# Performance work log

Measured on AMD Instinct MI355X. Metric: run time of the kernel, lower is better.

Reference implementation:

```python
import jax, jax.numpy as jnp
import numpy as np

B, L, C, K = 8, 16384, 64, 7
NORM_FACTOR = 1.0
LN_EPS = 1e-6


def setup_inputs() -> dict:
    key = jax.random.key(0)
    k0, k1, k2 = jax.random.split(key, 3)
    x = jax.random.normal(k0, (B, L, C), dtype=jnp.float32)
    # lecun_normal-style init for (C_out, C_in, K) dynamic-conv weights
    weights = jax.random.normal(k1, (C, C, K), dtype=jnp.float32) / np.float32(np.sqrt(C))
    ln_scale = jnp.ones((C,), dtype=jnp.float32)
    ln_bias = jnp.zeros((C,), dtype=jnp.float32)
    conv_kernel = jax.random.normal(k2, (C, C), dtype=jnp.float32) / np.float32(np.sqrt(C))
    conv_bias = jnp.zeros((C,), dtype=jnp.float32)
    prelu_slope = jnp.asarray(0.01, dtype=jnp.float32)
    return {"x": x, "weights": weights, "ln_scale": ln_scale, "ln_bias": ln_bias,
            "conv_kernel": conv_kernel, "conv_bias": conv_bias, "prelu_slope": prelu_slope}


def reference(x, weights, ln_scale, ln_bias, conv_kernel, conv_bias, prelu_slope):
    b, l, c = x.shape
    k = weights.shape[-1]
    x0 = x  # residual source, (B, L, C)

    # im2col unfold over sequence: window 2K, stride 2, no padding
    p = jax.lax.conv_general_dilated_patches(
        jnp.transpose(x, (0, 2, 1)),  # (B, C, L)
        filter_shape=(2 * k,), window_strides=(2,), padding=((0, 0),))
    t = p.shape[-1]  # out_len = (L - 2K)//2 + 1
    p = jnp.reshape(p, (b, c, 2 * k, t))
    p = jnp.transpose(p, (0, 1, 3, 2))  # (B, C, T, 2K)

    # dynamic weights from the trailing 2T inputs: (B, 2T, C) x (C, C, K) -> (B, C, 2T, K)
    w = jnp.einsum('blc,dck->bdlk', x0[:, -(t * 2):, :], weights)
    even_seq = w[:, :, ::2, :]   # (B, C, T, K)
    odd_seq = w[:, :, 1::2, :]   # (B, C, T, K)
    w = jnp.stack([even_seq, odd_seq], axis=-1)         # (B, C, T, K, 2)
    w = jnp.reshape(w, (b, c, t, k * 2))                # interleaved (B, C, T, 2K)
    w = jnp.tanh(w / NORM_FACTOR)

    # gated windowed sum
    y = jnp.sum(p * w, axis=3)          # (B, C, T)
    y = jnp.transpose(y, (0, 2, 1))     # (B, T, C)

    # inner skip: stride-2 subsample of input, aligned to the tail
    y = x0[:, ::2, :][:, -t:, :] + y

    # LayerNorm over channel dim (flax default eps=1e-6, with scale and bias)
    mu = jnp.mean(y, axis=-1, keepdims=True)
    var = jnp.mean(jnp.square(y - mu), axis=-1, keepdims=True)
    yn = (y - mu) * jax.lax.rsqrt(var + LN_EPS) * ln_scale + ln_bias

    # 1x1 conv + PReLU + outer skip
    z = jnp.einsum('btc,co->bto', yn, conv_kernel) + conv_bias
    z = jnp.where(z >= 0, z, prelu_slope * z)
    return yn + z
```

## Files before the change

### kernel.cpp

```cpp
#include <hip/hip_runtime.h>
#include <stdint.h>

#define BB 8
#define LLEN 16384
#define CC 64
#define TOUT 8186
#define TILE_T 32
#define NROWS 76
#define SXS 68
#define SXGS 72
#define YNS 66
#define YNBS 72

typedef __attribute__((ext_vector_type(8))) short short8;
typedef __attribute__((ext_vector_type(4))) float float4v;
typedef __attribute__((ext_vector_type(4))) unsigned short ushort4v;

__device__ inline unsigned short f2bf(float f) {
  union { float f; uint32_t u; } v; v.f = f;
  uint32_t r = v.u + 0x7fffu + ((v.u >> 16) & 1u);
  return (unsigned short)(r >> 16);
}
__device__ inline float rcp_fast(float x) {
  float r;
  asm("v_rcp_f32 %0, %1" : "=v"(r) : "v"(x));
  return r;
}
__device__ inline float tanh_fast(float a) {
  float e = __expf(2.0f * a);
  return 1.0f - 2.0f * rcp_fast(e + 1.0f);
}

__global__ void prep_frags(const float* __restrict__ weights,
                           const float* __restrict__ ck,
                           unsigned short* __restrict__ wfrag,
                           unsigned short* __restrict__ ckfrag)
{
  int bid = blockIdx.x, tid = threadIdx.x;
  if (bid < 56) {
    int nt = bid >> 1, kh = bid & 1;
    for (int e = tid; e < 512; e += 256) {
      int ln = e >> 3, j = e & 7;
      int kk = nt >> 2;
      int d  = (nt & 3) * 16 + (ln & 15);
      int cp = kh * 32 + (ln >> 4) * 8 + j;
      wfrag[(bid * 64 + ln) * 8 + j] = f2bf(weights[d * 448 + cp * 7 + kk]);
    }
  } else {
    int bb2 = bid - 56;
    int nt = bb2 >> 1, kh = bb2 & 1;
    for (int e = tid; e < 512; e += 256) {
      int ln = e >> 3, j = e & 7;
      int oo = nt * 16 + (ln & 15);
      int c2 = kh * 32 + (ln >> 4) * 8 + j;
      ckfrag[(bb2 * 64 + ln) * 8 + j] = f2bf(ck[c2 * 64 + oo]);
    }
  }
}

__global__ __launch_bounds__(256, 4)
void convblock_main(const float* __restrict__ x,
                    const unsigned short* __restrict__ wfrag,
                    const unsigned short* __restrict__ ckfrag,
                    const float* __restrict__ ln_scale,
                    const float* __restrict__ ln_bias,
                    const float* __restrict__ conv_bias,
                    const float* __restrict__ prelu_slope,
                    float* __restrict__ out)
{
  __shared__ __align__(16) char smem[29888];
  float*          sx2 = (float*)smem;
  unsigned short* ynb = (unsigned short*)smem;
  unsigned short* sxg = (unsigned short*)(smem + 20672);
  float*          ynf = (float*)(smem + 20672);

  const int tid  = threadIdx.x;
  const int b    = blockIdx.x >> 8;
  const int t0   = (blockIdx.x & 255) * TILE_T;
  const int lane = tid & 63;
  const int w    = tid >> 6;
  const int l15  = tid & 15;
  const int q    = (tid >> 4) & 3;

  {
    const float* xb = x + (size_t)b * ((size_t)LLEN * CC);
    #pragma unroll
    for (int i = 0; i < 5; ++i) {
      int idx = tid + i * 256;
      if (idx < NROWS * 16) {
        int row = idx >> 4, f4 = idx & 15, c0 = f4 * 4;
        int rowg = 2 * t0 + row;
        if (rowg > LLEN - 1) rowg = LLEN - 1;
        float4v v = *(const float4v*)(xb + (size_t)rowg * CC + c0);
        int base = row * SXS + 16 * (f4 & 3) + (f4 >> 2);
        sx2[base + 0]  = v[0];
        sx2[base + 4]  = v[1];
        sx2[base + 8]  = v[2];
        sx2[base + 12] = v[3];
        if (row >= 12) {
          ushort4v p;
          p[0] = f2bf(v[0]); p[1] = f2bf(v[1]); p[2] = f2bf(v[2]); p[3] = f2bf(v[3]);
          *(ushort4v*)&sxg[(row - 12) * SXGS + c0] = p;
        }
      }
    }
  }
  float lnS[4], lnB[4];
  #pragma unroll
  for (int dq = 0; dq < 4; ++dq) {
    lnS[dq] = ln_scale[16 * dq + l15];
    lnB[dq] = ln_bias[16 * dq + l15];
  }
  __syncthreads();

  short8 a0 = *(const short8*)&sxg[(16 * w + l15) * SXGS + q * 8];
  short8 a1 = *(const short8*)&sxg[(16 * w + l15) * SXGS + 32 + q * 8];
  __syncthreads();

  float y[2][4];
  #pragma unroll
  for (int dlt = 0; dlt < 2; ++dlt)
    #pragma unroll
    for (int dq = 0; dq < 4; ++dq) y[dlt][dq] = 0.f;

  const int dtbase = 8 * w + 2 * q;
  #pragma unroll
  for (int kk = 0; kk < 7; ++kk) {
    float4v acc[4];
    #pragma unroll
    for (int dq = 0; dq < 4; ++dq) {
      int nt = kk * 4 + dq;
      short8 b0 = *(const short8*)&wfrag[((nt * 2 + 0) * 64 + lane) * 8];
      short8 b1 = *(const short8*)&wfrag[((nt * 2 + 1) * 64 + lane) * 8];
      float4v a = (float4v){0.f, 0.f, 0.f, 0.f};
      a = __builtin_amdgcn_mfma_f32_16x16x32_bf16(a0, b0, a, 0, 0, 0);
      a = __builtin_amdgcn_mfma_f32_16x16x32_bf16(a1, b1, a, 0, 0, 0);
      acc[dq] = a;
    }
    #pragma unroll
    for (int dlt = 0; dlt < 2; ++dlt) {
      int rowe = 2 * (dtbase + dlt) + 2 * kk;
      float4v xe = *(const float4v*)&sx2[rowe * SXS + l15 * 4];
      float4v xo = *(const float4v*)&sx2[(rowe + 1) * SXS + l15 * 4];
      #pragma unroll
      for (int dq = 0; dq < 4; ++dq) {
        float ge = tanh_fast(acc[dq][2 * dlt + 0]);
        float go = tanh_fast(acc[dq][2 * dlt + 1]);
        y[dlt][dq] += xe[dq] * ge + xo[dq] * go;
        if (kk == 6) y[dlt][dq] += xe[dq];
      }
    }
  }

  float ynr[2][4];
  #pragma unroll
  for (int dlt = 0; dlt < 2; ++dlt) {
    float s1 = y[dlt][0] + y[dlt][1] + y[dlt][2] + y[dlt][3];
    float s2 = y[dlt][0]*y[dlt][0] + y[dlt][1]*y[dlt][1]
             + y[dlt][2]*y[dlt][2] + y[dlt][3]*y[dlt][3];
    #pragma unroll
    for (int m = 1; m < 16; m <<= 1) {
      s1 += __shfl_xor(s1, m, 64);
      s2 += __shfl_xor(s2, m, 64);
    }
    float mu   = s1 * (1.0f / 64.0f);
    float var  = s2 * (1.0f / 64.0f) - mu * mu;
    float rstd = rsqrtf(var + 1e-6f);
    int dt = dtbase + dlt;
    #pragma unroll
    for (int dq = 0; dq < 4; ++dq) {
      float yn = (y[dlt][dq] - mu) * rstd * lnS[dq] + lnB[dq];
      ynr[dlt][dq] = yn;
      ynf[dt * YNS + 16 * dq + l15] = yn;
    }
  }
  __syncthreads();

  #pragma unroll
  for (int dlt = 0; dlt < 2; ++dlt)
    #pragma unroll
    for (int dq = 0; dq < 4; ++dq)
      ynb[(dtbase + dlt) * YNBS + 16 * dq + l15] = f2bf(ynr[dlt][dq]);
  __syncthreads();

  const float sl = prelu_slope[0];
  const int   o  = 16 * w + l15;
  const float cb = conv_bias[o];
  short8 bf0 = *(const short8*)&ckfrag[((w * 2 + 0) * 64 + lane) * 8];
  short8 bf1 = *(const short8*)&ckfrag[((w * 2 + 1) * 64 + lane) * 8];
  #pragma unroll
  for (int mt = 0; mt < 2; ++mt) {
    short8 af0 = *(const short8*)&ynb[(mt * 16 + l15) * YNBS + q * 8];
    short8 af1 = *(const short8*)&ynb[(mt * 16 + l15) * YNBS + 32 + q * 8];
    float4v zc = (float4v){0.f, 0.f, 0.f, 0.f};
    zc = __builtin_amdgcn_mfma_f32_16x16x32_bf16(af0, bf0, zc, 0, 0, 0);
    zc = __builtin_amdgcn_mfma_f32_16x16x32_bf16(af1, bf1, zc, 0, 0, 0);
    #pragma unroll
    for (int r = 0; r < 4; ++r) {
      int t  = mt * 16 + 4 * q + r;
      int tg = t0 + t;
      if (tg < TOUT) {
        float z = zc[r] + cb;
        z = (z >= 0.f) ? z : sl * z;
        out[((size_t)b * TOUT + tg) * CC + o] = ynf[t * YNS + o] + z;
      }
    }
  }
}

extern "C" void kernel_launch(void* const* d_in, const int* in_sizes, int n_in,
                              void* d_out, int out_size, void* d_ws, size_t ws_size,
                              hipStream_t stream)
{
  const float* x        = (const float*)d_in[0];
  const float* weights  = (const float*)d_in[1];
  const float* ln_scale = (const float*)d_in[2];
  const float* ln_bias  = (const float*)d_in[3];
  const float* ck       = (const float*)d_in[4];
  const float* cb       = (const float*)d_in[5];
  const float* slope    = (const float*)d_in[6];
  unsigned short* wfrag  = (unsigned short*)d_ws;
  unsigned short* ckfrag = (unsigned short*)((char*)d_ws + 57344);

  prep_frags<<<64, 256, 0, stream>>>(weights, ck, wfrag, ckfrag);
  convblock_main<<<BB * 256, 256, 0, stream>>>(x, wfrag, ckfrag, ln_scale,
                                               ln_bias, cb, slope, (float*)d_out);
}
```

Before: 112.8 us.

## Double tile to 64 outputs, stage weight fragments in LDS, pack bf16 pairs

Doubles the per-block time tile to 64 outputs, so each weight fragment now feeds two MFMA row groups, which halves the global weight-fragment traffic per output. Weight fragments are prefetched into a double-buffered LDS area with direct global-to-LDS loads, with a barrier after each tap. The fp32 x window in LDS is replaced by packed bf16 even/odd pairs in an XOR-swizzled layout to cut LDS size and bank conflicts. The costs are lower gated-sum precision from bf16 x, more LDS per block and fewer blocks per SM (launch bounds drop from 4 to 3), plus seven extra barriers.

```diff
diff --git a/kernel.cpp b/kernel.cpp
--- a/kernel.cpp
+++ b/kernel.cpp
@@ -5,15 +5,17 @@
 #define LLEN 16384
 #define CC 64
 #define TOUT 8186
-#define TILE_T 32
-#define NROWS 76
-#define SXS 68
-#define SXGS 72
+#define TILE_T 64
+#define NROWS 140
+#define NPAIR 70
+#define SXPS 68
+#define SXGS 68
 #define YNS 66
-#define YNBS 72
+#define YNBS 76
 
 typedef __attribute__((ext_vector_type(8))) short short8;
 typedef __attribute__((ext_vector_type(4))) float float4v;
+typedef __attribute__((ext_vector_type(4))) unsigned int uint4v;
 typedef __attribute__((ext_vector_type(4))) unsigned short ushort4v;
 
 __device__ inline unsigned short f2bf(float f) {
@@ -22,13 +24,16 @@
   return (unsigned short)(r >> 16);
 }
 __device__ inline float rcp_fast(float x) {
-  float r;
-  asm("v_rcp_f32 %0, %1" : "=v"(r) : "v"(x));
-  return r;
+  float r; asm("v_rcp_f32 %0, %1" : "=v"(r) : "v"(x)); return r;
 }
 __device__ inline float tanh_fast(float a) {
   float e = __expf(2.0f * a);
   return 1.0f - 2.0f * rcp_fast(e + 1.0f);
+}
+__device__ inline void gload_lds16(const void* g, void* l) {
+  __builtin_amdgcn_global_load_lds(
+      (const __attribute__((address_space(1))) void*)g,
+      (__attribute__((address_space(3))) void*)l, 16, 0, 0);
 }
 
 __global__ void prep_frags(const float* __restrict__ weights,
@@ -58,7 +63,7 @@
   }
 }
 
-__global__ __launch_bounds__(256, 4)
+__global__ __launch_bounds__(256, 3)
 void convblock_main(const float* __restrict__ x,
                     const unsigned short* __restrict__ wfrag,
                     const unsigned short* __restrict__ ckfrag,
@@ -68,40 +73,53 @@
                     const float* __restrict__ prelu_slope,
                     float* __restrict__ out)
 {
-  __shared__ __align__(16) char smem[29888];
-  float*          sx2 = (float*)smem;
-  unsigned short* ynb = (unsigned short*)smem;
-  unsigned short* sxg = (unsigned short*)(smem + 20672);
-  float*          ynf = (float*)(smem + 20672);
+  __shared__ __align__(16) char smem[52832];
+  uint32_t*       sxp  = (uint32_t*)smem;
+  unsigned short* sxg  = (unsigned short*)(smem + 19040);
+  unsigned short* wbuf = (unsigned short*)(smem + 36448);
+  float*          ynf  = (float*)(smem + 19040);
+  unsigned short* ynb  = (unsigned short*)smem;
 
   const int tid  = threadIdx.x;
-  const int b    = blockIdx.x >> 8;
-  const int t0   = (blockIdx.x & 255) * TILE_T;
+  const int b    = blockIdx.x >> 7;
+  const int t0   = (blockIdx.x & 127) * TILE_T;
   const int lane = tid & 63;
   const int w    = tid >> 6;
   const int l15  = tid & 15;
   const int q    = (tid >> 4) & 3;
 
   {
+    const char* s0 = (const char*)wfrag + ((((0 * 4 + w) * 2 + 0) * 64 + lane) << 4);
+    const char* s1 = (const char*)wfrag + ((((0 * 4 + w) * 2 + 1) * 64 + lane) << 4);
+    gload_lds16(s0, (char*)wbuf + (w * 2 + 0) * 1024);
+    gload_lds16(s1, (char*)wbuf + (w * 2 + 1) * 1024);
+  }
+
+  {
     const float* xb = x + (size_t)b * ((size_t)LLEN * CC);
     #pragma unroll
     for (int i = 0; i < 5; ++i) {
-      int idx = tid + i * 256;
-      if (idx < NROWS * 16) {
-        int row = idx >> 4, f4 = idx & 15, c0 = f4 * 4;
-        int rowg = 2 * t0 + row;
-        if (rowg > LLEN - 1) rowg = LLEN - 1;
-        float4v v = *(const float4v*)(xb + (size_t)rowg * CC + c0);
-        int base = row * SXS + 16 * (f4 & 3) + (f4 >> 2);
-        sx2[base + 0]  = v[0];
-        sx2[base + 4]  = v[1];
-        sx2[base + 8]  = v[2];
-        sx2[base + 12] = v[3];
-        if (row >= 12) {
-          ushort4v p;
-          p[0] = f2bf(v[0]); p[1] = f2bf(v[1]); p[2] = f2bf(v[2]); p[3] = f2bf(v[3]);
-          *(ushort4v*)&sxg[(row - 12) * SXGS + c0] = p;
+      int u = tid + i * 256;
+      if (u < NPAIR * 16) {
+        int rp = u >> 4, f4 = u & 15, c0 = f4 * 4;
+        int g0 = 2 * t0 + 2 * rp, g1 = g0 + 1;
+        if (g0 > LLEN - 1) g0 = LLEN - 1;
+        if (g1 > LLEN - 1) g1 = LLEN - 1;
+        float4v ve = *(const float4v*)(xb + (size_t)g0 * CC + c0);
+        float4v vo = *(const float4v*)(xb + (size_t)g1 * CC + c0);
+        ushort4v pe, po;
+        #pragma unroll
+        for (int j = 0; j < 4; ++j) { pe[j] = f2bf(ve[j]); po[j] = f2bf(vo[j]); }
+        int sw = rp & 7;
+        #pragma unroll
+        for (int j = 0; j < 4; ++j) {
+          int c = c0 + j;
+          sxp[rp * SXPS + (((c & 15) ^ sw) << 2) + (c >> 4)] =
+              (uint32_t)pe[j] | ((uint32_t)po[j] << 16);
         }
+        int r0 = 2 * rp, r1 = 2 * rp + 1;
+        if (r0 >= 12) *(ushort4v*)&sxg[(r0 - 12) * SXGS + c0] = pe;
+        if (r1 >= 12) *(ushort4v*)&sxg[(r1 - 12) * SXGS + c0] = po;
       }
     }
   }
@@ -115,72 +133,87 @@
 
   short8 a0 = *(const short8*)&sxg[(16 * w + l15) * SXGS + q * 8];
   short8 a1 = *(const short8*)&sxg[(16 * w + l15) * SXGS + 32 + q * 8];
-  __syncthreads();
-
-  float y[2][4];
-  #pragma unroll
-  for (int dlt = 0; dlt < 2; ++dlt)
-    #pragma unroll
-    for (int dq = 0; dq < 4; ++dq) y[dlt][dq] = 0.f;
-
-  const int dtbase = 8 * w + 2 * q;
+  short8 a2 = *(const short8*)&sxg[(64 + 16 * w + l15) * SXGS + q * 8];
+  short8 a3 = *(const short8*)&sxg[(64 + 16 * w + l15) * SXGS + 32 + q * 8];
+
+  float y[2][2][4];
+  #pragma unroll
+  for (int ph = 0; ph < 2; ++ph)
+    #pragma unroll
+    for (int dlt = 0; dlt < 2; ++dlt)
+      #pragma unroll
+      for (int dq = 0; dq < 4; ++dq) y[ph][dlt][dq] = 0.f;
+
+  const int tb = 8 * w + 2 * q;
   #pragma unroll
   for (int kk = 0; kk < 7; ++kk) {
-    float4v acc[4];
+    if (kk < 6) {
+      const char* s0 = (const char*)wfrag + (((((kk + 1) * 4 + w) * 2 + 0) * 64 + lane) << 4);
+      const char* s1 = (const char*)wfrag + (((((kk + 1) * 4 + w) * 2 + 1) * 64 + lane) << 4);
+      char* db = (char*)wbuf + ((kk + 1) & 1) * 8192;
+      gload_lds16(s0, db + (w * 2 + 0) * 1024);
+      gload_lds16(s1, db + (w * 2 + 1) * 1024);
+    }
+    const unsigned short* wb = wbuf + (kk & 1) * 4096;
+    float4v acc[2][4];
     #pragma unroll
     for (int dq = 0; dq < 4; ++dq) {
-      int nt = kk * 4 + dq;
-      short8 b0 = *(const short8*)&wfrag[((nt * 2 + 0) * 64 + lane) * 8];
-      short8 b1 = *(const short8*)&wfrag[((nt * 2 + 1) * 64 + lane) * 8];
-      float4v a = (float4v){0.f, 0.f, 0.f, 0.f};
-      a = __builtin_amdgcn_mfma_f32_16x16x32_bf16(a0, b0, a, 0, 0, 0);
-      a = __builtin_amdgcn_mfma_f32_16x16x32_bf16(a1, b1, a, 0, 0, 0);
-      acc[dq] = a;
-    }
+      short8 b0 = *(const short8*)&wb[((dq * 2 + 0) * 64 + lane) * 8];
+      short8 b1 = *(const short8*)&wb[((dq * 2 + 1) * 64 + lane) * 8];
+      float4v u0 = (float4v){0.f, 0.f, 0.f, 0.f};
+      float4v u1 = (float4v){0.f, 0.f, 0.f, 0.f};
+      u0 = __builtin_amdgcn_mfma_f32_16x16x32_bf16(a0, b0, u0, 0, 0, 0);
+      u0 = __builtin_amdgcn_mfma_f32_16x16x32_bf16(a1, b1, u0, 0, 0, 0);
+      u1 = __builtin_amdgcn_mfma_f32_16x16x32_bf16(a2, b0, u1, 0, 0, 0);
+      u1 = __builtin_amdgcn_mfma_f32_16x16x32_bf16(a3, b1, u1, 0, 0, 0);
+      acc[0][dq] = u0;
+      acc[1][dq] = u1;
+    }
+    #pragma unroll
+    for (int ph = 0; ph < 2; ++ph) {
+      #pragma unroll
+      for (int dlt = 0; dlt < 2; ++dlt) {
+        int rp = ph * 32 + tb + dlt + kk;
+        uint4v pr = *(const uint4v*)&sxp[rp * SXPS + ((l15 ^ (rp & 7)) << 2)];
+        #pragma unroll
+        for (int dq = 0; dq < 4; ++dq) {
+          uint32_t u = pr[dq];
+          float xe = __uint_as_float(u << 16);
+          float xo = __uint_as_float(u & 0xffff0000u);
+          float ge = tanh_fast(acc[ph][dq][2 * dlt + 0]);
+          float go = tanh_fast(acc[ph][dq][2 * dlt + 1]);
+          y[ph][dlt][dq] += xe * ge + xo * go;
+          if (kk == 6) y[ph][dlt][dq] += xe;
+        }
+      }
+    }
+    __syncthreads();
+  }
+
+  #pragma unroll
+  for (int ph = 0; ph < 2; ++ph) {
     #pragma unroll
     for (int dlt = 0; dlt < 2; ++dlt) {
-      int rowe = 2 * (dtbase + dlt) + 2 * kk;
-      float4v xe = *(const float4v*)&sx2[rowe * SXS + l15 * 4];
-      float4v xo = *(const float4v*)&sx2[(rowe + 1) * SXS + l15 * 4];
+      float s1 = y[ph][dlt][0] + y[ph][dlt][1] + y[ph][dlt][2] + y[ph][dlt][3];
+      float s2 = y[ph][dlt][0]*y[ph][dlt][0] + y[ph][dlt][1]*y[ph][dlt][1]
+               + y[ph][dlt][2]*y[ph][dlt][2] + y[ph][dlt][3]*y[ph][dlt][3];
+      #pragma unroll
+      for (int m = 1; m < 16; m <<= 1) {
+        s1 += __shfl_xor(s1, m, 64);
+        s2 += __shfl_xor(s2, m, 64);
+      }
+      float mu   = s1 * (1.0f / 64.0f);
+      float var  = s2 * (1.0f / 64.0f) - mu * mu;
+      float rstd = rsqrtf(var + 1e-6f);
+      int tl = ph * 32 + tb + dlt;
       #pragma unroll
       for (int dq = 0; dq < 4; ++dq) {
-        float ge = tanh_fast(acc[dq][2 * dlt + 0]);
-        float go = tanh_fast(acc[dq][2 * dlt + 1]);
-        y[dlt][dq] += xe[dq] * ge + xo[dq] * go;
-        if (kk == 6) y[dlt][dq] += xe[dq];
-      }
-    }
-  }
-
-  float ynr[2][4];
-  #pragma unroll
-  for (int dlt = 0; dlt < 2; ++dlt) {
-    float s1 = y[dlt][0] + y[dlt][1] + y[dlt][2] + y[dlt][3];
-    float s2 = y[dlt][0]*y[dlt][0] + y[dlt][1]*y[dlt][1]
-             + y[dlt][2]*y[dlt][2] + y[dlt][3]*y[dlt][3];
-    #pragma unroll
-    for (int m = 1; m < 16; m <<= 1) {
-      s1 += __shfl_xor(s1, m, 64);
-      s2 += __shfl_xor(s2, m, 64);
-    }
-    float mu   = s1 * (1.0f / 64.0f);
-    float var  = s2 * (1.0f / 64.0f) - mu * mu;
-    float rstd = rsqrtf(var + 1e-6f);
-    int dt = dtbase + dlt;
-    #pragma unroll
-    for (int dq = 0; dq < 4; ++dq) {
-      float yn = (y[dlt][dq] - mu) * rstd * lnS[dq] + lnB[dq];
-      ynr[dlt][dq] = yn;
-      ynf[dt * YNS + 16 * dq + l15] = yn;
-    }
-  }
-  __syncthreads();
-
-  #pragma unroll
-  for (int dlt = 0; dlt < 2; ++dlt)
-    #pragma unroll
-    for (int dq = 0; dq < 4; ++dq)
-      ynb[(dtbase + dlt) * YNBS + 16 * dq + l15] = f2bf(ynr[dlt][dq]);
+        float yn = (y[ph][dlt][dq] - mu) * rstd * lnS[dq] + lnB[dq];
+        ynf[tl * YNS + 16 * dq + l15] = yn;
+        ynb[tl * YNBS + 16 * dq + l15] = f2bf(yn);
+      }
+    }
+  }
   __syncthreads();
 
   const float sl = prelu_slope[0];
@@ -189,7 +222,7 @@
   short8 bf0 = *(const short8*)&ckfrag[((w * 2 + 0) * 64 + lane) * 8];
   short8 bf1 = *(const short8*)&ckfrag[((w * 2 + 1) * 64 + lane) * 8];
   #pragma unroll
-  for (int mt = 0; mt < 2; ++mt) {
+  for (int mt = 0; mt < 4; ++mt) {
     short8 af0 = *(const short8*)&ynb[(mt * 16 + l15) * YNBS + q * 8];
     short8 af1 = *(const short8*)&ynb[(mt * 16 + l15) * YNBS + 32 + q * 8];
     float4v zc = (float4v){0.f, 0.f, 0.f, 0.f};
@@ -223,6 +256,6 @@
   unsigned short* ckfrag = (unsigned short*)((char*)d_ws + 57344);
 
   prep_frags<<<64, 256, 0, stream>>>(weights, ck, wfrag, ckfrag);
-  convblock_main<<<BB * 256, 256, 0, stream>>>(x, wfrag, ckfrag, ln_scale,
+  convblock_main<<<BB * 128, 256, 0, stream>>>(x, wfrag, ckfrag, ln_scale,
                                                ln_bias, cb, slope, (float*)d_out);
 }
```

Result: no change. 114.7 us (+1.7%).
